# Optimization experiments

Hardware: AMD Instinct MI355X
Metric: run time of the kernel (lower is better)

## Reference

```python
import jax, jax.numpy as jnp
import numpy as np

N_NODES = 50000
N_EDGES = 800000
D = 128


def setup_inputs() -> dict:
    key = jax.random.key(0)
    k1, k2, k3, k4 = jax.random.split(key, 4)
    x = jax.random.normal(k1, (N_NODES, D), dtype=jnp.float32)
    src = jax.random.randint(k2, (N_EDGES,), 0, N_NODES, dtype=jnp.int64)
    dst = jax.random.randint(k3, (N_EDGES,), 0, N_NODES, dtype=jnp.int64)
    # nn.Linear(D, D, bias=False): weight shape [out, in]
    W = jax.random.normal(k4, (D, D), dtype=jnp.float32) * (1.0 / np.sqrt(D))
    return {"x": x, "src": src, "dst": dst, "W": W}


def reference(x, src, dst, W):
    h_in = x
    # update_all(copy_src, reduce_sum): gather src features, segment-sum over dst
    agg = jax.ops.segment_sum(x[src], dst, num_segments=N_NODES)  # [N, D]
    h = agg @ W.T                 # Linear(bias=False)
    h = jax.nn.relu(h)            # activation
    h = h + h_in                  # residual (is_normalize=False)
    return h
```

## Files before the change

kernel.cpp:

```cpp
#include <hip/hip_runtime.h>
#include <hip/hip_bf16.h>

#define N_NODES 50000
#define N_EDGES 800000
#define D 128

#define NBUCK 782
#define BCAP  2048
#define LCAP  1536

#define SCAT_BLOCKS ((N_EDGES / 4 + 1023) / 1024)

using bf16x8 = __attribute__((ext_vector_type(8))) short;
using u16x8  = __attribute__((ext_vector_type(8))) unsigned short;
using f32x4  = __attribute__((ext_vector_type(4))) float;

static __device__ __forceinline__ ushort f2bf(float f) {
    __hip_bfloat16 h = __float2bfloat16(f);
    return *reinterpret_cast<ushort*>(&h);
}
static __device__ __forceinline__ float bf2f(ushort u) {
    return __uint_as_float(((unsigned)u) << 16);
}


__global__ void __launch_bounds__(1024)
convert_scatter(const float4* __restrict__ x4, ushort* __restrict__ xb,
                const int* __restrict__ src, const int* __restrict__ dst,
                int* __restrict__ bcnt, int* __restrict__ pairs) {
    __shared__ int lcnt[NBUCK], lbase[NBUCK];
    const int tid = threadIdx.x;
    if (tid < NBUCK) lcnt[tid] = 0;

    const int i = blockIdx.x * 1024 + tid;
    const bool valid = i < N_EDGES / 4;
    int4 s, d;
    if (valid) {
        s = ((const int4*)src)[i];
        d = ((const int4*)dst)[i];
    }

    const int total4 = N_NODES * D / 4;
    const int stride = gridDim.x * 1024;
    for (int j = blockIdx.x * 1024 + tid; j < total4; j += stride) {
        float4 v = x4[j];
        ushort4 u = make_ushort4(f2bf(v.x), f2bf(v.y), f2bf(v.z), f2bf(v.w));
        *(ushort4*)(xb + (size_t)j * 4) = u;
    }
    __syncthreads();

    int bkt[4], slot[4];
    if (valid) {
        bkt[0] = d.x >> 6; slot[0] = atomicAdd(&lcnt[bkt[0]], 1);
        bkt[1] = d.y >> 6; slot[1] = atomicAdd(&lcnt[bkt[1]], 1);
        bkt[2] = d.z >> 6; slot[2] = atomicAdd(&lcnt[bkt[2]], 1);
        bkt[3] = d.w >> 6; slot[3] = atomicAdd(&lcnt[bkt[3]], 1);
    }
    __syncthreads();
    if (tid < NBUCK) {
        int c = lcnt[tid];
        lbase[tid] = c ? atomicAdd(&bcnt[tid], c) : 0;
    }
    __syncthreads();
    if (valid) {
#pragma unroll
        for (int e = 0; e < 4; ++e) {
            int sv = (e == 0) ? s.x : (e == 1) ? s.y : (e == 2) ? s.z : s.w;
            int dv = (e == 0) ? d.x : (e == 1) ? d.y : (e == 2) ? d.z : d.w;
            int pos = lbase[bkt[e]] + slot[e];
            if (pos < BCAP)
                pairs[bkt[e] * BCAP + pos] = sv | ((dv & 63) << 16);
        }
    }
}

__global__ void __launch_bounds__(256)
csr_gather_gemm(const int* __restrict__ pairs, const int* __restrict__ bcnt,
                const ushort* __restrict__ xb, const float* __restrict__ W,
                float* __restrict__ out) {
    __shared__ __align__(16) char lds[54016];
    ushort* Wl    = (ushort*)lds;
    ushort* lsrc  = (ushort*)(lds + 32768);
    ushort* aggL  = (ushort*)(lds + 35840);
    int*    lcnt2 = (int*)(lds + 53248);
    int*    lcur  = (int*)(lds + 53504);
    int*    lbeg  = (int*)(lds + 53760);

    const int b    = blockIdx.x;
    const int tid  = threadIdx.x;
    const int lane = tid & 63;
    const int wv   = tid >> 6;
    const int m16  = lane & 15;
    const int q    = lane >> 4;

#pragma unroll
    for (int i = 0; i < 8; ++i) {
        int g  = tid + i * 256;
        int o  = g & 127;
        int kc = g >> 7;
        const float4* wp = (const float4*)(W + (size_t)o * D + kc * 8);
        float4 w0 = wp[0], w1 = wp[1];
        bf16x8 hv;
        hv[0] = (short)f2bf(w0.x); hv[1] = (short)f2bf(w0.y);
        hv[2] = (short)f2bf(w0.z); hv[3] = (short)f2bf(w0.w);
        hv[4] = (short)f2bf(w1.x); hv[5] = (short)f2bf(w1.y);
        hv[6] = (short)f2bf(w1.z); hv[7] = (short)f2bf(w1.w);
        *(bf16x8*)&Wl[g * 8] = hv;
    }

    const int base = b * BCAP;
    int n = bcnt[b];
    if (n > LCAP) n = LCAP;
    if (tid < 64) lcnt2[tid] = 0;
    __syncthreads();
    for (int i = tid; i < n; i += 256)
        atomicAdd(&lcnt2[pairs[base + i] >> 16], 1);
    __syncthreads();
    if (tid < 64) {
        int v = lcnt2[tid];
        int incl = v;
#pragma unroll
        for (int o = 1; o < 64; o <<= 1) {
            int t = __shfl_up(incl, o, 64);
            if (tid >= o) incl += t;
        }
        lbeg[tid] = incl - v;
        lcur[tid] = incl - v;
    }
    __syncthreads();
    for (int i = tid; i < n; i += 256) {
        int p = pairs[base + i];
        int pos = atomicAdd(&lcur[p >> 16], 1);
        lsrc[pos] = (ushort)(p & 0xFFFF);
    }
    __syncthreads();

    const int c8 = m16 << 3;
    const ushort* xbb = xb + c8;
#pragma unroll 1
    for (int m = 0; m < 16; ++m) {
        const int node = wv * 16 + m;
        const int beg = lbeg[node], end = lcur[node];
        float acc[8];
#pragma unroll
        for (int j = 0; j < 8; ++j) acc[j] = 0.f;

        int t = beg;
        for (; t + 16 <= end; t += 16) {
            int s0 = lsrc[t + q];
            int s1 = lsrc[t + 4 + q];
            int s2 = lsrc[t + 8 + q];
            int s3 = lsrc[t + 12 + q];
            u16x8 u0 = *(const u16x8*)(xbb + (size_t)s0 * D);
            u16x8 u1 = *(const u16x8*)(xbb + (size_t)s1 * D);
            u16x8 u2 = *(const u16x8*)(xbb + (size_t)s2 * D);
            u16x8 u3 = *(const u16x8*)(xbb + (size_t)s3 * D);
#pragma unroll
            for (int j = 0; j < 8; ++j)
                acc[j] += (bf2f(u0[j]) + bf2f(u1[j])) + (bf2f(u2[j]) + bf2f(u3[j]));
        }
        for (; t + 4 <= end; t += 4) {
            int s = lsrc[t + q];
            u16x8 u = *(const u16x8*)(xbb + (size_t)s * D);
#pragma unroll
            for (int j = 0; j < 8; ++j) acc[j] += bf2f(u[j]);
        }
        const int rem = end - t;
        if (rem && q < rem) {
            int s = lsrc[t + q];
            u16x8 u = *(const u16x8*)(xbb + (size_t)s * D);
#pragma unroll
            for (int j = 0; j < 8; ++j) acc[j] += bf2f(u[j]);
        }
#pragma unroll
        for (int j = 0; j < 8; ++j) {
            acc[j] += __shfl_xor(acc[j], 16, 64);
            acc[j] += __shfl_xor(acc[j], 32, 64);
        }
        if (q == 0) {
            u16x8 u;
#pragma unroll
            for (int j = 0; j < 8; ++j) u[j] = f2bf(acc[j]);
            *(u16x8*)&aggL[(size_t)node * 136 + c8] = u;
        }
    }
    __syncthreads();

    bf16x8 a[4];
#pragma unroll
    for (int kb = 0; kb < 4; ++kb)
        a[kb] = *(const bf16x8*)&aggL[(size_t)(wv * 16 + m16) * 136 + kb * 32 + q * 8];

    f32x4 acc[8];
#pragma unroll
    for (int t = 0; t < 8; ++t) {
        acc[t] = (f32x4){0.f, 0.f, 0.f, 0.f};
#pragma unroll
        for (int kb = 0; kb < 4; ++kb) {
            bf16x8 bfr = *(const bf16x8*)&Wl[(((kb * 4 + q) * 128) + t * 16 + m16) * 8];
            acc[t] = __builtin_amdgcn_mfma_f32_16x16x32_bf16(a[kb], bfr, acc[t], 0, 0, 0);
        }
    }

    __syncthreads();
    float* Ew = (float*)(lds + wv * 8448);
#pragma unroll
    for (int t = 0; t < 8; ++t)
#pragma unroll
        for (int r = 0; r < 4; ++r)
            Ew[(q * 4 + r) * 132 + t * 16 + m16] = acc[t][r];

    const int nb = b * 64 + wv * 16;
    const int h  = lane >> 5;
    const int c4 = (lane & 31) << 2;
#pragma unroll
    for (int j = 0; j < 8; ++j) {
        int r = j * 2 + h;
        int node = nb + r;
        if (node < N_NODES) {
            float4 v  = *(const float4*)&Ew[r * 132 + c4];
            ushort4 xu = *(const ushort4*)(xb + (size_t)node * D + c4);
            float4 o;
            o.x = fmaxf(v.x, 0.f) + bf2f(xu.x);
            o.y = fmaxf(v.y, 0.f) + bf2f(xu.y);
            o.z = fmaxf(v.z, 0.f) + bf2f(xu.z);
            o.w = fmaxf(v.w, 0.f) + bf2f(xu.w);
            *(float4*)(out + (size_t)node * D + c4) = o;
        }
    }
}

__global__ void zero_out(float4* __restrict__ p, int n4) {
    int i = blockIdx.x * 256 + threadIdx.x;
    if (i < n4) p[i] = make_float4(0.f, 0.f, 0.f, 0.f);
}
__global__ void scatter_edges(const float* __restrict__ x,
                              const int* __restrict__ src,
                              const int* __restrict__ dst,
                              float* __restrict__ agg) {
    long long tid = (long long)blockIdx.x * 256 + threadIdx.x;
    if (tid >= (long long)N_EDGES * 32) return;
    int edge = (int)(tid >> 5);
    int c    = ((int)tid & 31) << 2;
    const float4 v = *(const float4*)(x + (size_t)src[edge] * D + c);
    float* p = agg + (size_t)dst[edge] * D + c;
    unsafeAtomicAdd(p + 0, v.x);
    unsafeAtomicAdd(p + 1, v.y);
    unsafeAtomicAdd(p + 2, v.z);
    unsafeAtomicAdd(p + 3, v.w);
}
__global__ void __launch_bounds__(256)
gemm_relu_res_f32(float* data, const float* __restrict__ W,
                  const float* __restrict__ x) {
    __shared__ __align__(16) char lds[50176];
    ushort* Wl = (ushort*)lds;
    ushort* Al = (ushort*)(lds + 32768);
    const int tid  = threadIdx.x;
    const int lane = tid & 63;
    const int wv   = tid >> 6;
    const int m16  = lane & 15;
    const int q    = lane >> 4;
#pragma unroll
    for (int i = 0; i < 8; ++i) {
        int g  = tid + i * 256;
        int o  = g & 127;
        int kc = g >> 7;
        const float4* wp = (const float4*)(W + (size_t)o * D + kc * 8);
        float4 w0 = wp[0], w1 = wp[1];
        bf16x8 hv;
        hv[0] = (short)f2bf(w0.x); hv[1] = (short)f2bf(w0.y);
        hv[2] = (short)f2bf(w0.z); hv[3] = (short)f2bf(w0.w);
        hv[4] = (short)f2bf(w1.x); hv[5] = (short)f2bf(w1.y);
        hv[6] = (short)f2bf(w1.z); hv[7] = (short)f2bf(w1.w);
        *(bf16x8*)&Wl[g * 8] = hv;
    }
    __syncthreads();
    const int nb = blockIdx.x * 64 + wv * 16;
    ushort* Aw = &Al[wv * (16 * 136)];
#pragma unroll
    for (int m = 0; m < 16; ++m) {
        int node = nb + m;
        float2 v = make_float2(0.f, 0.f);
        if (node < N_NODES)
            v = *(const float2*)(data + (size_t)node * D + lane * 2);
        *(ushort2*)&Aw[m * 136 + lane * 2] = make_ushort2(f2bf(v.x), f2bf(v.y));
    }
    bf16x8 a[4];
#pragma unroll
    for (int kb = 0; kb < 4; ++kb)
        a[kb] = *(const bf16x8*)&Aw[m16 * 136 + kb * 32 + q * 8];
    f32x4 acc[8];
#pragma unroll
    for (int t = 0; t < 8; ++t) {
        acc[t] = (f32x4){0.f, 0.f, 0.f, 0.f};
#pragma unroll
        for (int kb = 0; kb < 4; ++kb) {
            bf16x8 bfr = *(const bf16x8*)&Wl[(((kb * 4 + q) * 128) + t * 16 + m16) * 8];
            acc[t] = __builtin_amdgcn_mfma_f32_16x16x32_bf16(a[kb], bfr, acc[t], 0, 0, 0);
        }
    }
    __syncthreads();
    float* Ew = (float*)(lds + wv * 8448);
#pragma unroll
    for (int t = 0; t < 8; ++t)
#pragma unroll
        for (int r = 0; r < 4; ++r)
            Ew[(q * 4 + r) * 132 + t * 16 + m16] = acc[t][r];
    const int h  = lane >> 5;
    const int c4 = (lane & 31) << 2;
#pragma unroll
    for (int j = 0; j < 8; ++j) {
        int r = j * 2 + h;
        int node = nb + r;
        if (node < N_NODES) {
            float4 v  = *(const float4*)&Ew[r * 132 + c4];
            float4 xi = *(const float4*)(x + (size_t)node * D + c4);
            float4 o;
            o.x = fmaxf(v.x, 0.f) + xi.x;
            o.y = fmaxf(v.y, 0.f) + xi.y;
            o.z = fmaxf(v.z, 0.f) + xi.z;
            o.w = fmaxf(v.w, 0.f) + xi.w;
            *(float4*)(data + (size_t)node * D + c4) = o;
        }
    }
}

extern "C" void kernel_launch(void* const* d_in, const int* in_sizes, int n_in,
                              void* d_out, int out_size, void* d_ws, size_t ws_size,
                              hipStream_t stream) {
    const float* x   = (const float*)d_in[0];
    const int*   src = (const int*)d_in[1];
    const int*   dst = (const int*)d_in[2];
    const float* W   = (const float*)d_in[3];
    float* out = (float*)d_out;

    char* ws = (char*)d_ws;
    int*    bcnt  = (int*)ws;        ws += (size_t)NBUCK * 4;
    ws = (char*)(((uintptr_t)ws + 15) & ~(uintptr_t)15);
    int*    pairs = (int*)ws;        ws += (size_t)NBUCK * BCAP * 4;
    ushort* xb    = (ushort*)ws;     ws += (size_t)N_NODES * D * 2;
    const bool big_ws = (ws_size >= (size_t)(ws - (char*)d_ws));

    if (big_ws) {
        hipMemsetAsync(bcnt, 0, (size_t)NBUCK * 4, stream);
        convert_scatter<<<SCAT_BLOCKS, 1024, 0, stream>>>(
            (const float4*)x, xb, src, dst, bcnt, pairs);
        csr_gather_gemm<<<NBUCK, 256, 0, stream>>>(pairs, bcnt, xb, W, out);
    } else {
        int n4 = N_NODES * D / 4;
        zero_out<<<(n4 + 255) / 256, 256, 0, stream>>>((float4*)out, n4);
        long long n_scatter = (long long)N_EDGES * 32;
        scatter_edges<<<(int)((n_scatter + 255) / 256), 256, 0, stream>>>(
            x, src, dst, out);
        gemm_relu_res_f32<<<(N_NODES + 63) / 64, 256, 0, stream>>>(out, W, x);
    }
}
```

Baseline: 163.4 us.

## Shrink buckets to 16 nodes, pre-convert W to bf16 once, cut LDS

Buckets now cover 16 destination nodes instead of 64, so the gather+GEMM kernel launches 3125 small blocks with far less LDS (about 14KB instead of 54KB), which allows more resident blocks per CU. W is converted to bf16 once in the scatter kernel and read from global memory rather than being re-converted into LDS by every block. Each wave now computes two output column tiles for 16 nodes instead of all tiles for its own 16 nodes. In exchange, W fragments are read straight from global/L2 on every block, the per-bucket cap drops to 512 edges, and per-block LDS histogram overhead grows in the scatter kernel.

```diff
diff --git a/kernel.cpp b/kernel.cpp
--- a/kernel.cpp
+++ b/kernel.cpp
@@ -5,9 +5,8 @@
 #define N_EDGES 800000
 #define D 128
 
-#define NBUCK 782
-#define BCAP  2048
-#define LCAP  1536
+#define NBUCK 3125
+#define BCAP  512
 
 #define SCAT_BLOCKS ((N_EDGES / 4 + 1023) / 1024)
 
@@ -26,11 +25,12 @@
 
 __global__ void __launch_bounds__(1024)
 convert_scatter(const float4* __restrict__ x4, ushort* __restrict__ xb,
+                const float* __restrict__ W, ushort* __restrict__ wb,
                 const int* __restrict__ src, const int* __restrict__ dst,
                 int* __restrict__ bcnt, int* __restrict__ pairs) {
     __shared__ int lcnt[NBUCK], lbase[NBUCK];
     const int tid = threadIdx.x;
-    if (tid < NBUCK) lcnt[tid] = 0;
+    for (int t0 = tid; t0 < NBUCK; t0 += 1024) lcnt[t0] = 0;
 
     const int i = blockIdx.x * 1024 + tid;
     const bool valid = i < N_EDGES / 4;
@@ -40,62 +40,8 @@
         d = ((const int4*)dst)[i];
     }
 
-    const int total4 = N_NODES * D / 4;
-    const int stride = gridDim.x * 1024;
-    for (int j = blockIdx.x * 1024 + tid; j < total4; j += stride) {
-        float4 v = x4[j];
-        ushort4 u = make_ushort4(f2bf(v.x), f2bf(v.y), f2bf(v.z), f2bf(v.w));
-        *(ushort4*)(xb + (size_t)j * 4) = u;
-    }
-    __syncthreads();
-
-    int bkt[4], slot[4];
-    if (valid) {
-        bkt[0] = d.x >> 6; slot[0] = atomicAdd(&lcnt[bkt[0]], 1);
-        bkt[1] = d.y >> 6; slot[1] = atomicAdd(&lcnt[bkt[1]], 1);
-        bkt[2] = d.z >> 6; slot[2] = atomicAdd(&lcnt[bkt[2]], 1);
-        bkt[3] = d.w >> 6; slot[3] = atomicAdd(&lcnt[bkt[3]], 1);
-    }
-    __syncthreads();
-    if (tid < NBUCK) {
-        int c = lcnt[tid];
-        lbase[tid] = c ? atomicAdd(&bcnt[tid], c) : 0;
-    }
-    __syncthreads();
-    if (valid) {
-#pragma unroll
-        for (int e = 0; e < 4; ++e) {
-            int sv = (e == 0) ? s.x : (e == 1) ? s.y : (e == 2) ? s.z : s.w;
-            int dv = (e == 0) ? d.x : (e == 1) ? d.y : (e == 2) ? d.z : d.w;
-            int pos = lbase[bkt[e]] + slot[e];
-            if (pos < BCAP)
-                pairs[bkt[e] * BCAP + pos] = sv | ((dv & 63) << 16);
-        }
-    }
-}
-
-__global__ void __launch_bounds__(256)
-csr_gather_gemm(const int* __restrict__ pairs, const int* __restrict__ bcnt,
-                const ushort* __restrict__ xb, const float* __restrict__ W,
-                float* __restrict__ out) {
-    __shared__ __align__(16) char lds[54016];
-    ushort* Wl    = (ushort*)lds;
-    ushort* lsrc  = (ushort*)(lds + 32768);
-    ushort* aggL  = (ushort*)(lds + 35840);
-    int*    lcnt2 = (int*)(lds + 53248);
-    int*    lcur  = (int*)(lds + 53504);
-    int*    lbeg  = (int*)(lds + 53760);
-
-    const int b    = blockIdx.x;
-    const int tid  = threadIdx.x;
-    const int lane = tid & 63;
-    const int wv   = tid >> 6;
-    const int m16  = lane & 15;
-    const int q    = lane >> 4;
-
-#pragma unroll
-    for (int i = 0; i < 8; ++i) {
-        int g  = tid + i * 256;
+    const int g = blockIdx.x * 1024 + tid;
+    if (g < 2048) {
         int o  = g & 127;
         int kc = g >> 7;
         const float4* wp = (const float4*)(W + (size_t)o * D + kc * 8);
@@ -105,22 +51,75 @@
         hv[2] = (short)f2bf(w0.z); hv[3] = (short)f2bf(w0.w);
         hv[4] = (short)f2bf(w1.x); hv[5] = (short)f2bf(w1.y);
         hv[6] = (short)f2bf(w1.z); hv[7] = (short)f2bf(w1.w);
-        *(bf16x8*)&Wl[g * 8] = hv;
-    }
+        *(bf16x8*)&wb[g * 8] = hv;
+    }
+
+    const int total4 = N_NODES * D / 4;
+    const int stride = gridDim.x * 1024;
+    for (int j = blockIdx.x * 1024 + tid; j < total4; j += stride) {
+        float4 v = x4[j];
+        ushort4 u = make_ushort4(f2bf(v.x), f2bf(v.y), f2bf(v.z), f2bf(v.w));
+        *(ushort4*)(xb + (size_t)j * 4) = u;
+    }
+    __syncthreads();
+
+    int bkt[4], slot[4];
+    if (valid) {
+        bkt[0] = d.x >> 4; slot[0] = atomicAdd(&lcnt[bkt[0]], 1);
+        bkt[1] = d.y >> 4; slot[1] = atomicAdd(&lcnt[bkt[1]], 1);
+        bkt[2] = d.z >> 4; slot[2] = atomicAdd(&lcnt[bkt[2]], 1);
+        bkt[3] = d.w >> 4; slot[3] = atomicAdd(&lcnt[bkt[3]], 1);
+    }
+    __syncthreads();
+    for (int t0 = tid; t0 < NBUCK; t0 += 1024) {
+        int c = lcnt[t0];
+        lbase[t0] = c ? atomicAdd(&bcnt[t0], c) : 0;
+    }
+    __syncthreads();
+    if (valid) {
+#pragma unroll
+        for (int e = 0; e < 4; ++e) {
+            int sv = (e == 0) ? s.x : (e == 1) ? s.y : (e == 2) ? s.z : s.w;
+            int dv = (e == 0) ? d.x : (e == 1) ? d.y : (e == 2) ? d.z : d.w;
+            int pos = lbase[bkt[e]] + slot[e];
+            if (pos < BCAP)
+                pairs[bkt[e] * BCAP + pos] = sv | ((dv & 15) << 16);
+        }
+    }
+}
+
+__global__ void __launch_bounds__(256)
+csr_gather_gemm(const int* __restrict__ pairs, const int* __restrict__ bcnt,
+                const ushort* __restrict__ xb, const ushort* __restrict__ wb,
+                float* __restrict__ out) {
+    __shared__ __align__(16) char lds[14016];
+    ushort* lsrc  = (ushort*)lds;
+    ushort* aggL  = (ushort*)(lds + 1024);
+    float*  Ew    = (float*)(lds + 5376);
+    int*    lcnt2 = (int*)(lds + 13824);
+    int*    lcur  = (int*)(lds + 13888);
+    int*    lbeg  = (int*)(lds + 13952);
+
+    const int b    = blockIdx.x;
+    const int tid  = threadIdx.x;
+    const int lane = tid & 63;
+    const int wv   = tid >> 6;
+    const int m16  = lane & 15;
+    const int q    = lane >> 4;
 
     const int base = b * BCAP;
     int n = bcnt[b];
-    if (n > LCAP) n = LCAP;
-    if (tid < 64) lcnt2[tid] = 0;
+    if (n > BCAP) n = BCAP;
+    if (tid < 16) lcnt2[tid] = 0;
     __syncthreads();
     for (int i = tid; i < n; i += 256)
         atomicAdd(&lcnt2[pairs[base + i] >> 16], 1);
     __syncthreads();
-    if (tid < 64) {
+    if (tid < 16) {
         int v = lcnt2[tid];
         int incl = v;
 #pragma unroll
-        for (int o = 1; o < 64; o <<= 1) {
+        for (int o = 1; o < 16; o <<= 1) {
             int t = __shfl_up(incl, o, 64);
             if (tid >= o) incl += t;
         }
@@ -138,9 +137,9 @@
     const int c8 = m16 << 3;
     const ushort* xbb = xb + c8;
 #pragma unroll 1
-    for (int m = 0; m < 16; ++m) {
-        const int node = wv * 16 + m;
-        const int beg = lbeg[node], end = lcur[node];
+    for (int m = 0; m < 4; ++m) {
+        const int nloc = wv * 4 + m;
+        const int beg = lbeg[nloc], end = lcur[nloc];
         float acc[8];
 #pragma unroll
         for (int j = 0; j < 8; ++j) acc[j] = 0.f;
@@ -181,7 +180,7 @@
             u16x8 u;
 #pragma unroll
             for (int j = 0; j < 8; ++j) u[j] = f2bf(acc[j]);
-            *(u16x8*)&aggL[(size_t)node * 136 + c8] = u;
+            *(u16x8*)&aggL[(size_t)nloc * 136 + c8] = u;
         }
     }
     __syncthreads();
@@ -189,44 +188,43 @@
     bf16x8 a[4];
 #pragma unroll
     for (int kb = 0; kb < 4; ++kb)
-        a[kb] = *(const bf16x8*)&aggL[(size_t)(wv * 16 + m16) * 136 + kb * 32 + q * 8];
-
-    f32x4 acc[8];
-#pragma unroll
-    for (int t = 0; t < 8; ++t) {
-        acc[t] = (f32x4){0.f, 0.f, 0.f, 0.f};
+        a[kb] = *(const bf16x8*)&aggL[(size_t)m16 * 136 + kb * 32 + q * 8];
+
+    f32x4 acc[2];
+#pragma unroll
+    for (int tt = 0; tt < 2; ++tt) {
+        const int t = wv * 2 + tt;
+        acc[tt] = (f32x4){0.f, 0.f, 0.f, 0.f};
 #pragma unroll
         for (int kb = 0; kb < 4; ++kb) {
-            bf16x8 bfr = *(const bf16x8*)&Wl[(((kb * 4 + q) * 128) + t * 16 + m16) * 8];
-            acc[t] = __builtin_amdgcn_mfma_f32_16x16x32_bf16(a[kb], bfr, acc[t], 0, 0, 0);
-        }
-    }
-
-    __syncthreads();
-    float* Ew = (float*)(lds + wv * 8448);
-#pragma unroll
-    for (int t = 0; t < 8; ++t)
+            bf16x8 bfr = *(const bf16x8*)&wb[(((kb * 4 + q) * 128) + t * 16 + m16) * 8];
+            acc[tt] = __builtin_amdgcn_mfma_f32_16x16x32_bf16(a[kb], bfr, acc[tt], 0, 0, 0);
+        }
+    }
+
+#pragma unroll
+    for (int tt = 0; tt < 2; ++tt) {
+        const int t = wv * 2 + tt;
 #pragma unroll
         for (int r = 0; r < 4; ++r)
-            Ew[(q * 4 + r) * 132 + t * 16 + m16] = acc[t][r];
-
-    const int nb = b * 64 + wv * 16;
-    const int h  = lane >> 5;
-    const int c4 = (lane & 31) << 2;
-#pragma unroll
-    for (int j = 0; j < 8; ++j) {
-        int r = j * 2 + h;
-        int node = nb + r;
-        if (node < N_NODES) {
-            float4 v  = *(const float4*)&Ew[r * 132 + c4];
-            ushort4 xu = *(const ushort4*)(xb + (size_t)node * D + c4);
-            float4 o;
-            o.x = fmaxf(v.x, 0.f) + bf2f(xu.x);
-            o.y = fmaxf(v.y, 0.f) + bf2f(xu.y);
-            o.z = fmaxf(v.z, 0.f) + bf2f(xu.z);
-            o.w = fmaxf(v.w, 0.f) + bf2f(xu.w);
-            *(float4*)(out + (size_t)node * D + c4) = o;
-        }
+            Ew[(q * 4 + r) * 132 + t * 16 + m16] = acc[tt][r];
+    }
+    __syncthreads();
+
+#pragma unroll
+    for (int k = 0; k < 2; ++k) {
+        int idx = tid + k * 256;
+        int row = idx >> 5;
+        int c4  = (idx & 31) << 2;
+        int node = b * 16 + row;
+        float4 v  = *(const float4*)&Ew[row * 132 + c4];
+        ushort4 xu = *(const ushort4*)(xb + (size_t)node * D + c4);
+        float4 o;
+        o.x = fmaxf(v.x, 0.f) + bf2f(xu.x);
+        o.y = fmaxf(v.y, 0.f) + bf2f(xu.y);
+        o.z = fmaxf(v.z, 0.f) + bf2f(xu.z);
+        o.w = fmaxf(v.w, 0.f) + bf2f(xu.w);
+        *(float4*)(out + (size_t)node * D + c4) = o;
     }
 }
 
@@ -339,13 +337,14 @@
     ws = (char*)(((uintptr_t)ws + 15) & ~(uintptr_t)15);
     int*    pairs = (int*)ws;        ws += (size_t)NBUCK * BCAP * 4;
     ushort* xb    = (ushort*)ws;     ws += (size_t)N_NODES * D * 2;
+    ushort* wb    = (ushort*)ws;     ws += (size_t)D * D * 2;
     const bool big_ws = (ws_size >= (size_t)(ws - (char*)d_ws));
 
     if (big_ws) {
         hipMemsetAsync(bcnt, 0, (size_t)NBUCK * 4, stream);
         convert_scatter<<<SCAT_BLOCKS, 1024, 0, stream>>>(
-            (const float4*)x, xb, src, dst, bcnt, pairs);
-        csr_gather_gemm<<<NBUCK, 256, 0, stream>>>(pairs, bcnt, xb, W, out);
+            (const float4*)x, xb, W, wb, src, dst, bcnt, pairs);
+        csr_gather_gemm<<<NBUCK, 256, 0, stream>>>(pairs, bcnt, xb, wb, out);
     } else {
         int n4 = N_NODES * D / 4;
         zero_out<<<(n4 + 255) / 256, 256, 0, stream>>>((float4*)out, n4);
```

Measured after the change: 137.3 us. 1.19x faster.
